# Optimization experiments

Measured on AMD Instinct MI355X. Metric: run time of the kernel, lower is better.

## Reference

```python
import jax, jax.numpy as jnp
import numpy as np

N_NODES = 50000
N_EDGES = 800000
IN_DIM = 128
EDGE_DIM = 32
HID = 64


def _glorot(key, shape):
    fan_in, fan_out = shape[0], shape[1]
    lim = float(np.sqrt(6.0 / (fan_in + fan_out)))
    return jax.random.uniform(key, shape, jnp.float32, -lim, lim)


def setup_inputs() -> dict:
    key = jax.random.key(0)
    ks = jax.random.split(key, 16)
    x = jax.random.normal(ks[0], (N_NODES, IN_DIM), jnp.float32)
    edge_index = jax.random.randint(ks[1], (2, N_EDGES), 0, N_NODES, jnp.int64)
    edge_attr = jax.random.normal(ks[2], (N_EDGES, EDGE_DIM), jnp.float32)
    message = jax.random.normal(ks[3], (N_EDGES, HID), jnp.float32)
    return {
        "x": x,
        "edge_index": edge_index,
        "edge_attr": edge_attr,
        "message": message,
        "W_src": _glorot(ks[4], (IN_DIM, HID)),
        "W_dest": _glorot(ks[5], (IN_DIM, HID)),
        "W_edge": _glorot(ks[6], (EDGE_DIM, HID)),
        "attn_vec": _glorot(ks[7], (1, HID)),
        "mlp_w1": _glorot(ks[8], (2 * HID, HID)),
        "mlp_b1": jnp.zeros((HID,), jnp.float32),
        "bn1_g": jnp.ones((HID,), jnp.float32),
        "bn1_b": jnp.zeros((HID,), jnp.float32),
        "mlp_w2": _glorot(ks[9], (HID, HID)),
        "mlp_b2": jnp.zeros((HID,), jnp.float32),
        "bn2_g": jnp.ones((HID,), jnp.float32),
        "bn2_b": jnp.zeros((HID,), jnp.float32),
        "amlp_w": _glorot(ks[10], (HID, 1)),
        "amlp_b": jnp.zeros((1,), jnp.float32),
    }


def _batchnorm(h, g, b, eps=1e-5):
    mu = jnp.mean(h, axis=0)
    var = jnp.var(h, axis=0)  # biased, as torch BN training forward
    return (h - mu) * jax.lax.rsqrt(var + eps) * g + b


def _segment_softmax(scores, seg, num_segments):
    m = jax.ops.segment_max(scores, seg, num_segments=num_segments)
    m = jnp.where(jnp.isneginf(m), 0.0, m)
    e = jnp.exp(scores - m[seg])
    s = jax.ops.segment_sum(e, seg, num_segments=num_segments)
    return e / s[seg]


def _scatter_max0(vals, seg, num_segments):
    # torch_scatter reduce='max' fills empty segments with 0
    out = jax.ops.segment_max(vals, seg, num_segments=num_segments)
    return jnp.where(jnp.isneginf(out), 0.0, out)


def reference(x, edge_index, edge_attr, message, W_src, W_dest, W_edge, attn_vec,
              mlp_w1, mlp_b1, bn1_g, bn1_b, mlp_w2, mlp_b2, bn2_g, bn2_b,
              amlp_w, amlp_b):
    row, col = edge_index[0], edge_index[1]
    # attention scores per edge
    h = x[row] @ W_src + x[col] @ W_dest + edge_attr @ W_edge  # [E, H]
    scores = jax.nn.leaky_relu(h @ attn_vec[0], negative_slope=0.2)  # [E]
    attn = _segment_softmax(scores, col, N_NODES)  # [E]
    msg = message * attn[:, None]  # [E, H]
    fwd = _scatter_max0(msg, col, N_NODES)  # [N, H]
    bwd = _scatter_max0(msg, row, N_NODES)  # [N, H]
    out = jnp.concatenate([fwd, bwd], axis=1)  # [N, 2H]
    # node MLP (BatchNorm in training-stats mode, dropout disabled)
    h1 = jax.nn.relu(_batchnorm(out @ mlp_w1 + mlp_b1, bn1_g, bn1_b))
    h2 = jax.nn.relu(_batchnorm(h1 @ mlp_w2 + mlp_b2, bn2_g, bn2_b))
    gate = jax.nn.sigmoid(h2 @ amlp_w + amlp_b).reshape(-1)  # [N]
    return h2, gate
```

## Files before the change

### kernel.cpp

```cpp
#include <hip/hip_runtime.h>
#include <hip/hip_bf16.h>
#include <float.h>

#define IN_DIM 128
#define EDGE_DIM 32
#define HID 64
#define BKT_G 64
#define BCAP 3072
#define NBKT_MAX 784
#define CHUNK 4096

__global__ void k_uvw(const float* __restrict__ Wsrc, const float* __restrict__ Wdst,
                      const float* __restrict__ Wedge, const float* __restrict__ avec,
                      const int* __restrict__ ei32, int* sflag,
                      float* u, float* v, float* w,
                      int* gcur, float* stats, int nbkt) {
    int gt = blockIdx.x * blockDim.x + threadIdx.x;
    int gstride = gridDim.x * blockDim.x;
    for (int i = gt; i < 2 * nbkt; i += gstride) gcur[i] = 0;
    for (int i = gt; i < 512; i += gstride) stats[i] = 0.0f;
    if (gt == 0) {
        int odd_or = ei32[1] | ei32[3] | ei32[5] | ei32[7] | ei32[9] | ei32[11];
        sflag[0] = (odd_or == 0) ? 2 : 1;
    }
    int wave = gt >> 6;
    int lane = threadIdx.x & 63;
    const float* src; float* dst; int row;
    if (wave < 128)      { src = Wsrc;  dst = u; row = wave; }
    else if (wave < 256) { src = Wdst;  dst = v; row = wave - 128; }
    else if (wave < 288) { src = Wedge; dst = w; row = wave - 256; }
    else return;
    float acc = src[row * HID + lane] * avec[lane];
    for (int o = 32; o >= 1; o >>= 1) acc += __shfl_xor(acc, o);
    if (lane == 0) dst[row] = acc;
}

__global__ void k_pqdot(const float* __restrict__ x, const float* __restrict__ u,
                        const float* __restrict__ v,
                        const float* __restrict__ ea, const float* __restrict__ w,
                        float* p, float* q, float* rdot, int N, int E, int pqBlocks) {
    if ((int)blockIdx.x < pqBlocks) {
        int wave = (blockIdx.x * blockDim.x + threadIdx.x) >> 6;
        int lane = threadIdx.x & 63;
        if (wave >= N) return;
        const float* xr = x + (size_t)wave * IN_DIM;
        float a0 = xr[lane], a1 = xr[lane + 64];
        float pp = a0 * u[lane] + a1 * u[lane + 64];
        float qq = a0 * v[lane] + a1 * v[lane + 64];
        for (int m = 32; m >= 1; m >>= 1) { pp += __shfl_xor(pp, m); qq += __shfl_xor(qq, m); }
        if (lane == 0) { p[wave] = pp; q[wave] = qq; }
    } else {
        int gid = (blockIdx.x - pqBlocks) * blockDim.x + threadIdx.x;
        int e = gid >> 3;
        int j = gid & 7;
        if (e >= E) return;
        float4 av = ((const float4*)ea)[(size_t)e * 8 + j];
        float4 wv = ((const float4*)w)[j];
        float val = av.x * wv.x + av.y * wv.y + av.z * wv.z + av.w * wv.w;
        val += __shfl_xor(val, 4);
        val += __shfl_xor(val, 2);
        val += __shfl_xor(val, 1);
        if (j == 0) rdot[e] = val;
    }
}

__global__ __launch_bounds__(256) void k_binscore(const int* __restrict__ ei,
                                                  const int* __restrict__ sflag,
                                                  const float* __restrict__ rdot,
                                                  const float* __restrict__ p,
                                                  const float* __restrict__ q,
                                                  float* scores,
                                                  int* gcur_col, int* gcur_row,
                                                  unsigned* bbuf_col, unsigned* bbuf_row,
                                                  int E, int nbkt) {
    __shared__ int lc[NBKT_MAX], lrw[NBKT_MAX];
    __shared__ int gc[NBKT_MAX], grw[NBKT_MAX];
    int tid = threadIdx.x;
    int e0 = blockIdx.x * CHUNK;
    int e1 = e0 + CHUNK; if (e1 > E) e1 = E;
    for (int i = tid; i < nbkt; i += 256) { lc[i] = 0; lrw[i] = 0; }
    __syncthreads();
    int st = sflag[0];
    for (int e = e0 + tid; e < e1; e += 256) {
        int r = ei[(size_t)st * e];
        int c = ei[(size_t)st * (E + e)];
        float sc = rdot[e] + p[r] + q[c];
        scores[e] = (sc > 0.f) ? sc : 0.2f * sc;
        atomicAdd(&lc[c >> 6], 1);
        atomicAdd(&lrw[r >> 6], 1);
    }
    __syncthreads();
    for (int b = tid; b < nbkt; b += 256) {
        int n1 = lc[b];  if (n1) gc[b]  = atomicAdd(&gcur_col[b], n1);
        int n2 = lrw[b]; if (n2) grw[b] = atomicAdd(&gcur_row[b], n2);
        lc[b] = 0; lrw[b] = 0;
    }
    __syncthreads();
    for (int e = e0 + tid; e < e1; e += 256) {
        int r = ei[(size_t)st * e];
        int c = ei[(size_t)st * (E + e)];
        int pos = gc[c >> 6] + atomicAdd(&lc[c >> 6], 1);
        if (pos < BCAP) bbuf_col[(size_t)(c >> 6) * BCAP + pos] = (unsigned)((e << 6) | (c & 63));
        int pos2 = grw[r >> 6] + atomicAdd(&lrw[r >> 6], 1);
        if (pos2 < BCAP) bbuf_row[(size_t)(r >> 6) * BCAP + pos2] = (unsigned)((e << 6) | (r & 63));
    }
}

__global__ __launch_bounds__(512) void k_sortfwd(float* scores, const float* __restrict__ msg,
                                                 const int* __restrict__ bcur,
                                                 const unsigned* __restrict__ bbuf,
                                                 float* fwd, int N) {
    __shared__ unsigned raw[BCAP];
    __shared__ unsigned srt[BCAP];
    __shared__ float    ssc[BCAP];
    __shared__ int cnt[BKT_G], cur[BKT_G], sstart[BKT_G + 1];
    int b = blockIdx.x, tid = threadIdx.x;
    int M = bcur[b]; if (M > BCAP) M = BCAP;
    if (tid < BKT_G) cnt[tid] = 0;
    __syncthreads();
    for (int i = tid; i < M; i += 512) {
        unsigned v = bbuf[(size_t)b * BCAP + i];
        raw[i] = v;
        atomicAdd(&cnt[v & 63], 1);
    }
    __syncthreads();
    if (tid < BKT_G) {
        int val = cnt[tid];
        int inc = val;
        for (int off = 1; off < BKT_G; off <<= 1) {
            int o = __shfl_up(inc, off);
            if (tid >= off) inc += o;
        }
        sstart[tid + 1] = inc;
        if (tid == 0) sstart[0] = 0;
        cur[tid] = inc - val;
    }
    __syncthreads();
    for (int j = tid; j < M; j += 512) {
        unsigned v = raw[j];
        int posn = atomicAdd(&cur[v & 63], 1);
        srt[posn] = v;
    }
    __syncthreads();
    for (int i = tid; i < M; i += 512) ssc[i] = scores[srt[i] >> 6];
    __syncthreads();
    int wave = tid >> 6, lane = tid & 63;
    for (int n = wave; n < BKT_G; n += 8) {
        int node = b * BKT_G + n;
        if (node >= N) continue;
        int a0 = sstart[n], len = sstart[n + 1] - a0;
        if (len == 0) { fwd[(size_t)node * HID + lane] = 0.f; continue; }
        float m = -FLT_MAX;
        for (int k = lane; k < len; k += 64) m = fmaxf(m, ssc[a0 + k]);
        for (int o = 32; o >= 1; o >>= 1) m = fmaxf(m, __shfl_xor(m, o));
        float ssum = 0.f;
        for (int k = lane; k < len; k += 64) ssum += expf(ssc[a0 + k] - m);
        for (int o = 32; o >= 1; o >>= 1) ssum += __shfl_xor(ssum, o);
        float rcp = 1.f / ssum;
        for (int k = lane; k < len; k += 64) {
            int i = a0 + k;
            float at = expf(ssc[i] - m) * rcp;
            ssc[i] = at;
            scores[srt[i] >> 6] = at;
        }
        asm volatile("s_waitcnt lgkmcnt(0)" ::: "memory");
        float acc = -FLT_MAX;
        int k = 0;
        for (; k + 8 <= len; k += 8) {
            float vv[8];
#pragma unroll
            for (int u8 = 0; u8 < 8; u8++) {
                int i = a0 + k + u8;
                vv[u8] = msg[(size_t)(srt[i] >> 6) * HID + lane] * ssc[i];
            }
#pragma unroll
            for (int u8 = 0; u8 < 8; u8++) acc = fmaxf(acc, vv[u8]);
        }
        for (; k < len; k++) {
            int i = a0 + k;
            acc = fmaxf(acc, msg[(size_t)(srt[i] >> 6) * HID + lane] * ssc[i]);
        }
        fwd[(size_t)node * HID + lane] = acc;
    }
}

__global__ __launch_bounds__(512) void k_sortbwd(const float* __restrict__ scores,
                                                 const float* __restrict__ msg,
                                                 const int* __restrict__ bcur,
                                                 const unsigned* __restrict__ bbuf,
                                                 float* bwd, int N) {
    __shared__ unsigned raw[BCAP];
    __shared__ unsigned srt[BCAP];
    __shared__ float    ssc[BCAP];
    __shared__ int cnt[BKT_G], cur[BKT_G], sstart[BKT_G + 1];
    int b = blockIdx.x, tid = threadIdx.x;
    int M = bcur[b]; if (M > BCAP) M = BCAP;
    if (tid < BKT_G) cnt[tid] = 0;
    __syncthreads();
    for (int i = tid; i < M; i += 512) {
        unsigned v = bbuf[(size_t)b * BCAP + i];
        raw[i] = v;
        atomicAdd(&cnt[v & 63], 1);
    }
    __syncthreads();
    if (tid < BKT_G) {
        int val = cnt[tid];
        int inc = val;
        for (int off = 1; off < BKT_G; off <<= 1) {
            int o = __shfl_up(inc, off);
            if (tid >= off) inc += o;
        }
        sstart[tid + 1] = inc;
        if (tid == 0) sstart[0] = 0;
        cur[tid] = inc - val;
    }
    __syncthreads();
    for (int j = tid; j < M; j += 512) {
        unsigned v = raw[j];
        int posn = atomicAdd(&cur[v & 63], 1);
        srt[posn] = v;
    }
    __syncthreads();
    for (int i = tid; i < M; i += 512) ssc[i] = scores[srt[i] >> 6];
    __syncthreads();
    int wave = tid >> 6, lane = tid & 63;
    for (int n = wave; n < BKT_G; n += 8) {
        int node = b * BKT_G + n;
        if (node >= N) continue;
        int a0 = sstart[n], len = sstart[n + 1] - a0;
        if (len == 0) { bwd[(size_t)node * HID + lane] = 0.f; continue; }
        float acc = -FLT_MAX;
        int k = 0;
        for (; k + 8 <= len; k += 8) {
            float vv[8];
#pragma unroll
            for (int u8 = 0; u8 < 8; u8++) {
                int i = a0 + k + u8;
                vv[u8] = msg[(size_t)(srt[i] >> 6) * HID + lane] * ssc[i];
            }
#pragma unroll
            for (int u8 = 0; u8 < 8; u8++) acc = fmaxf(acc, vv[u8]);
        }
        for (; k < len; k++) {
            int i = a0 + k;
            acc = fmaxf(acc, msg[(size_t)(srt[i] >> 6) * HID + lane] * ssc[i]);
        }
        bwd[(size_t)node * HID + lane] = acc;
    }
}

__global__ __launch_bounds__(256) void k_mlp1(const float* __restrict__ fwd,
                                              const float* __restrict__ bwd,
                                              const float* __restrict__ W1,
                                              const float* __restrict__ b1,
                                              float* pre1, float* gsum, float* gss, int N) {
    __shared__ float lsum[HID], lss[HID];
    int t = threadIdx.x;
    if (t < HID) { lsum[t] = 0.f; lss[t] = 0.f; }
    __syncthreads();
    int h = t & 63, lr = t >> 6;
    float bh = b1[h];
    float s = 0.f, ssq = 0.f;
    for (int n = blockIdx.x * 4 + lr; n < N; n += gridDim.x * 4) {
        const float* fr = fwd + (size_t)n * HID;
        const float* br = bwd + (size_t)n * HID;
        float a0 = bh, a1 = 0.f, a2 = 0.f, a3 = 0.f;
#pragma unroll
        for (int k = 0; k < HID; k += 4) {
            a0 += fr[k]     * W1[k * HID + h];
            a1 += fr[k + 1] * W1[(k + 1) * HID + h];
            a2 += fr[k + 2] * W1[(k + 2) * HID + h];
            a3 += fr[k + 3] * W1[(k + 3) * HID + h];
        }
#pragma unroll
        for (int k = 0; k < HID; k += 4) {
            a0 += br[k]     * W1[(HID + k) * HID + h];
            a1 += br[k + 1] * W1[(HID + k + 1) * HID + h];
            a2 += br[k + 2] * W1[(HID + k + 2) * HID + h];
            a3 += br[k + 3] * W1[(HID + k + 3) * HID + h];
        }
        float acc = (a0 + a1) + (a2 + a3);
        pre1[(size_t)n * HID + h] = acc;
        s += acc; ssq += acc * acc;
    }
    atomicAdd(&lsum[h], s);
    atomicAdd(&lss[h], ssq);
    __syncthreads();
    if (t < HID) { atomicAdd(&gsum[t], lsum[t]); atomicAdd(&gss[t], lss[t]); }
}

__global__ __launch_bounds__(256) void k_mlp2(const float* __restrict__ pre1,
                                              const float* __restrict__ gsum1,
                                              const float* __restrict__ gss1,
                                              const float* __restrict__ g1,
                                              const float* __restrict__ bb1,
                                              const float* __restrict__ W2,
                                              const float* __restrict__ b2v,
                                              float* pre2, float* gsum, float* gss, int N) {
    __shared__ float lsum[HID], lss[HID];
    __shared__ float sc1[HID], sh1[HID];
    int t = threadIdx.x;
    if (t < HID) {
        lsum[t] = 0.f; lss[t] = 0.f;
        float invN = 1.0f / (float)N;
        float mu = gsum1[t] * invN;
        float var = gss1[t] * invN - mu * mu;
        float rs = rsqrtf(var + 1e-5f);
        float s1 = rs * g1[t];
        sc1[t] = s1;
        sh1[t] = bb1[t] - mu * s1;
    }
    __syncthreads();
    int h = t & 63, lr = t >> 6;
    float bh = b2v[h];
    float s = 0.f, ssq = 0.f;
    for (int n = blockIdx.x * 4 + lr; n < N; n += gridDim.x * 4) {
        const float* pr = pre1 + (size_t)n * HID;
        float a0 = bh, a1 = 0.f, a2 = 0.f, a3 = 0.f;
#pragma unroll
        for (int k = 0; k < HID; k += 4) {
            float z0 = pr[k]     * sc1[k]     + sh1[k];     z0 = (z0 > 0.f) ? z0 : 0.f;
            float z1 = pr[k + 1] * sc1[k + 1] + sh1[k + 1]; z1 = (z1 > 0.f) ? z1 : 0.f;
            float z2 = pr[k + 2] * sc1[k + 2] + sh1[k + 2]; z2 = (z2 > 0.f) ? z2 : 0.f;
            float z3 = pr[k + 3] * sc1[k + 3] + sh1[k + 3]; z3 = (z3 > 0.f) ? z3 : 0.f;
            a0 += z0 * W2[k * HID + h];
            a1 += z1 * W2[(k + 1) * HID + h];
            a2 += z2 * W2[(k + 2) * HID + h];
            a3 += z3 * W2[(k + 3) * HID + h];
        }
        float acc = (a0 + a1) + (a2 + a3);
        pre2[(size_t)n * HID + h] = acc;
        s += acc; ssq += acc * acc;
    }
    atomicAdd(&lsum[h], s);
    atomicAdd(&lss[h], ssq);
    __syncthreads();
    if (t < HID) { atomicAdd(&gsum[t], lsum[t]); atomicAdd(&gss[t], lss[t]); }
}

__global__ __launch_bounds__(256) void k_out(const float* __restrict__ pre2,
                                             const float* __restrict__ gsum2,
                                             const float* __restrict__ gss2,
                                             const float* __restrict__ g2,
                                             const float* __restrict__ bb2,
                                             const float* __restrict__ amw,
                                             const float* __restrict__ amb,
                                             float* out, int N) {
    __shared__ float sc2[HID], sh2[HID];
    int t = threadIdx.x;
    if (t < HID) {
        float invN = 1.0f / (float)N;
        float mu = gsum2[t] * invN;
        float var = gss2[t] * invN - mu * mu;
        float rs = rsqrtf(var + 1e-5f);
        float s2 = rs * g2[t];
        sc2[t] = s2;
        sh2[t] = bb2[t] - mu * s2;
    }
    __syncthreads();
    int gid = blockIdx.x * blockDim.x + t;
    int n = gid >> 6, h = gid & 63;
    if (n >= N) return;
    float z = pre2[(size_t)n * HID + h] * sc2[h] + sh2[h];
    float h2 = (z > 0.f) ? z : 0.f;
    out[(size_t)n * HID + h] = h2;
    float part = h2 * amw[h];
    for (int m = 32; m >= 1; m >>= 1) part += __shfl_xor(part, m);
    if (h == 0) {
        float gate = 1.0f / (1.0f + expf(-(part + amb[0])));
        out[(size_t)N * HID + n] = gate;
    }
}

extern "C" void kernel_launch(void* const* d_in, const int* in_sizes, int n_in,
                              void* d_out, int out_size, void* d_ws, size_t ws_size,
                              hipStream_t stream) {
    const float* x     = (const float*)d_in[0];
    const int*   ei    = (const int*)d_in[1];
    const float* ea    = (const float*)d_in[2];
    const float* msg   = (const float*)d_in[3];
    const float* Wsrc  = (const float*)d_in[4];
    const float* Wdst  = (const float*)d_in[5];
    const float* Wedge = (const float*)d_in[6];
    const float* avec  = (const float*)d_in[7];
    const float* W1    = (const float*)d_in[8];
    const float* b1    = (const float*)d_in[9];
    const float* g1    = (const float*)d_in[10];
    const float* bb1   = (const float*)d_in[11];
    const float* W2    = (const float*)d_in[12];
    const float* b2    = (const float*)d_in[13];
    const float* g2    = (const float*)d_in[14];
    const float* bb2   = (const float*)d_in[15];
    const float* amw   = (const float*)d_in[16];
    const float* amb   = (const float*)d_in[17];
    float* out = (float*)d_out;

    const int N = in_sizes[0] / IN_DIM;
    const int E = in_sizes[1] / 2;
    const int NH = N * HID;
    const int nbkt = (N + BKT_G - 1) / BKT_G;

    float* ws = (float*)d_ws;
    float* gsum1  = ws;
    float* gss1   = ws + 64;
    float* gsum2  = ws + 128;
    float* gss2   = ws + 192;
    int*   sflag  = (int*)(ws + 512);
    float* u      = ws + 576;
    float* v      = ws + 704;
    float* w      = ws + 832;
    float* T        = ws + 1024;
    float* p        = T;
    float* q        = p + N;
    float* scores   = q + N;
    float* rdot     = scores + E;
    int*   gcur_col = (int*)(rdot + E);
    int*   gcur_row = gcur_col + nbkt;
    unsigned* bbuf_col = (unsigned*)(gcur_row + nbkt);
    unsigned* bbuf_row = bbuf_col + (size_t)nbkt * BCAP;
    size_t T_words  = 2 * (size_t)N + 2 * (size_t)E + 2 * (size_t)nbkt
                    + 2 * (size_t)nbkt * BCAP;
    size_t T_sz     = (T_words < (size_t)NH) ? (size_t)NH : T_words;
    float* fwd  = ws + 1024 + T_sz;
    float* bwd  = fwd + (size_t)NH;
    float* pre1 = T;
    float* pre2 = fwd;

    const int pqBlocks   = (N * 64 + 255) / 256;
    const int edotBlocks = (E * 8 + 255) / 256;

    hipLaunchKernelGGL(k_uvw, dim3(72), dim3(256), 0, stream,
                       Wsrc, Wdst, Wedge, avec, ei, sflag, u, v, w,
                       gcur_col, ws, nbkt);
    hipLaunchKernelGGL(k_pqdot, dim3(pqBlocks + edotBlocks), dim3(256), 0, stream,
                       x, u, v, ea, w, p, q, rdot, N, E, pqBlocks);
    hipLaunchKernelGGL(k_binscore, dim3((E + CHUNK - 1) / CHUNK), dim3(256), 0, stream,
                       ei, sflag, rdot, p, q, scores,
                       gcur_col, gcur_row, bbuf_col, bbuf_row, E, nbkt);
    hipLaunchKernelGGL(k_sortfwd, dim3(nbkt), dim3(512), 0, stream,
                       scores, msg, gcur_col, bbuf_col, fwd, N);
    hipLaunchKernelGGL(k_sortbwd, dim3(nbkt), dim3(512), 0, stream,
                       scores, msg, gcur_row, bbuf_row, bwd, N);
    hipLaunchKernelGGL(k_mlp1, dim3(1024), dim3(256), 0, stream,
                       fwd, bwd, W1, b1, pre1, gsum1, gss1, N);
    hipLaunchKernelGGL(k_mlp2, dim3(1024), dim3(256), 0, stream,
                       pre1, gsum1, gss1, g1, bb1, W2, b2, pre2, gsum2, gss2, N);
    hipLaunchKernelGGL(k_out, dim3(pqBlocks), dim3(256), 0, stream,
                       pre2, gsum2, gss2, g2, bb2, amw, amb, out, N);
}
```

Before: 307.8 us.

## Replace per-node sequential max with LDS atomicMax accumulation over bucket edges

The scatter-max in the forward and backward kernels now walks all edges of a 64-node bucket in a flat, wave-strided loop. It accumulates per-node maxima in a shared-memory array with order-preserving float-to-uint encoding and atomicMax, instead of each wave walking one node's sorted edge list. This removes load imbalance from variable node degree and drops the local counting sort in the backward kernel. In exchange it adds LDS atomics, which may contend, plus 16KB more shared memory per block, which can lower occupancy.

Measured after the change: 322.4 us. +4.8%, slower.

```diff
diff --git a/kernel.cpp b/kernel.cpp
--- a/kernel.cpp
+++ b/kernel.cpp
@@ -9,6 +9,16 @@
 #define BCAP 3072
 #define NBKT_MAX 784
 #define CHUNK 4096
+#define ENC_NEG_INF 0x007FFFFFu
+
+__device__ __forceinline__ unsigned encf(float f) {
+    unsigned u = __float_as_uint(f);
+    return (u & 0x80000000u) ? ~u : (u | 0x80000000u);
+}
+__device__ __forceinline__ float dec0(unsigned u) {
+    if (u == ENC_NEG_INF) return 0.0f;
+    return (u & 0x80000000u) ? __uint_as_float(u ^ 0x80000000u) : __uint_as_float(~u);
+}
 
 __global__ void k_uvw(const float* __restrict__ Wsrc, const float* __restrict__ Wdst,
                       const float* __restrict__ Wedge, const float* __restrict__ avec,
@@ -113,6 +123,7 @@
     __shared__ unsigned raw[BCAP];
     __shared__ unsigned srt[BCAP];
     __shared__ float    ssc[BCAP];
+    __shared__ unsigned facc[BKT_G * HID];
     __shared__ int cnt[BKT_G], cur[BKT_G], sstart[BKT_G + 1];
     int b = blockIdx.x, tid = threadIdx.x;
     int M = bcur[b]; if (M > BCAP) M = BCAP;
@@ -123,6 +134,7 @@
         raw[i] = v;
         atomicAdd(&cnt[v & 63], 1);
     }
+    for (int i = tid; i < BKT_G * HID; i += 512) facc[i] = ENC_NEG_INF;
     __syncthreads();
     if (tid < BKT_G) {
         int val = cnt[tid];
@@ -146,10 +158,8 @@
     __syncthreads();
     int wave = tid >> 6, lane = tid & 63;
     for (int n = wave; n < BKT_G; n += 8) {
-        int node = b * BKT_G + n;
-        if (node >= N) continue;
         int a0 = sstart[n], len = sstart[n + 1] - a0;
-        if (len == 0) { fwd[(size_t)node * HID + lane] = 0.f; continue; }
+        if (len == 0) continue;
         float m = -FLT_MAX;
         for (int k = lane; k < len; k += 64) m = fmaxf(m, ssc[a0 + k]);
         for (int o = 32; o >= 1; o >>= 1) m = fmaxf(m, __shfl_xor(m, o));
@@ -163,24 +173,30 @@
             ssc[i] = at;
             scores[srt[i] >> 6] = at;
         }
-        asm volatile("s_waitcnt lgkmcnt(0)" ::: "memory");
-        float acc = -FLT_MAX;
-        int k = 0;
-        for (; k + 8 <= len; k += 8) {
-            float vv[8];
-#pragma unroll
-            for (int u8 = 0; u8 < 8; u8++) {
-                int i = a0 + k + u8;
-                vv[u8] = msg[(size_t)(srt[i] >> 6) * HID + lane] * ssc[i];
-            }
-#pragma unroll
-            for (int u8 = 0; u8 < 8; u8++) acc = fmaxf(acc, vv[u8]);
-        }
-        for (; k < len; k++) {
-            int i = a0 + k;
-            acc = fmaxf(acc, msg[(size_t)(srt[i] >> 6) * HID + lane] * ssc[i]);
-        }
-        fwd[(size_t)node * HID + lane] = acc;
+    }
+    __syncthreads();
+    int i = wave;
+    for (; i + 24 < M; i += 32) {
+        unsigned s0 = srt[i], s1 = srt[i + 8], s2 = srt[i + 16], s3 = srt[i + 24];
+        float a0 = ssc[i], a1 = ssc[i + 8], a2 = ssc[i + 16], a3 = ssc[i + 24];
+        float v0 = msg[(size_t)(s0 >> 6) * HID + lane] * a0;
+        float v1 = msg[(size_t)(s1 >> 6) * HID + lane] * a1;
+        float v2 = msg[(size_t)(s2 >> 6) * HID + lane] * a2;
+        float v3 = msg[(size_t)(s3 >> 6) * HID + lane] * a3;
+        atomicMax(&facc[(s0 & 63) * HID + lane], encf(v0));
+        atomicMax(&facc[(s1 & 63) * HID + lane], encf(v1));
+        atomicMax(&facc[(s2 & 63) * HID + lane], encf(v2));
+        atomicMax(&facc[(s3 & 63) * HID + lane], encf(v3));
+    }
+    for (; i < M; i += 8) {
+        unsigned s0 = srt[i];
+        float v0 = msg[(size_t)(s0 >> 6) * HID + lane] * ssc[i];
+        atomicMax(&facc[(s0 & 63) * HID + lane], encf(v0));
+    }
+    __syncthreads();
+    for (int idx = tid; idx < BKT_G * HID; idx += 512) {
+        int node = b * BKT_G + (idx >> 6);
+        if (node < N) fwd[(size_t)node * HID + (idx & 63)] = dec0(facc[idx]);
     }
 }
 
@@ -190,62 +206,38 @@
                                                  const unsigned* __restrict__ bbuf,
                                                  float* bwd, int N) {
     __shared__ unsigned raw[BCAP];
-    __shared__ unsigned srt[BCAP];
     __shared__ float    ssc[BCAP];
-    __shared__ int cnt[BKT_G], cur[BKT_G], sstart[BKT_G + 1];
+    __shared__ unsigned facc[BKT_G * HID];
     int b = blockIdx.x, tid = threadIdx.x;
     int M = bcur[b]; if (M > BCAP) M = BCAP;
-    if (tid < BKT_G) cnt[tid] = 0;
-    __syncthreads();
-    for (int i = tid; i < M; i += 512) {
-        unsigned v = bbuf[(size_t)b * BCAP + i];
-        raw[i] = v;
-        atomicAdd(&cnt[v & 63], 1);
-    }
-    __syncthreads();
-    if (tid < BKT_G) {
-        int val = cnt[tid];
-        int inc = val;
-        for (int off = 1; off < BKT_G; off <<= 1) {
-            int o = __shfl_up(inc, off);
-            if (tid >= off) inc += o;
-        }
-        sstart[tid + 1] = inc;
-        if (tid == 0) sstart[0] = 0;
-        cur[tid] = inc - val;
-    }
-    __syncthreads();
-    for (int j = tid; j < M; j += 512) {
-        unsigned v = raw[j];
-        int posn = atomicAdd(&cur[v & 63], 1);
-        srt[posn] = v;
-    }
-    __syncthreads();
-    for (int i = tid; i < M; i += 512) ssc[i] = scores[srt[i] >> 6];
+    for (int i = tid; i < M; i += 512) raw[i] = bbuf[(size_t)b * BCAP + i];
+    for (int i = tid; i < BKT_G * HID; i += 512) facc[i] = ENC_NEG_INF;
+    __syncthreads();
+    for (int i = tid; i < M; i += 512) ssc[i] = scores[raw[i] >> 6];
     __syncthreads();
     int wave = tid >> 6, lane = tid & 63;
-    for (int n = wave; n < BKT_G; n += 8) {
-        int node = b * BKT_G + n;
-        if (node >= N) continue;
-        int a0 = sstart[n], len = sstart[n + 1] - a0;
-        if (len == 0) { bwd[(size_t)node * HID + lane] = 0.f; continue; }
-        float acc = -FLT_MAX;
-        int k = 0;
-        for (; k + 8 <= len; k += 8) {
-            float vv[8];
-#pragma unroll
-            for (int u8 = 0; u8 < 8; u8++) {
-                int i = a0 + k + u8;
-                vv[u8] = msg[(size_t)(srt[i] >> 6) * HID + lane] * ssc[i];
-            }
-#pragma unroll
-            for (int u8 = 0; u8 < 8; u8++) acc = fmaxf(acc, vv[u8]);
-        }
-        for (; k < len; k++) {
-            int i = a0 + k;
-            acc = fmaxf(acc, msg[(size_t)(srt[i] >> 6) * HID + lane] * ssc[i]);
-        }
-        bwd[(size_t)node * HID + lane] = acc;
+    int i = wave;
+    for (; i + 24 < M; i += 32) {
+        unsigned s0 = raw[i], s1 = raw[i + 8], s2 = raw[i + 16], s3 = raw[i + 24];
+        float a0 = ssc[i], a1 = ssc[i + 8], a2 = ssc[i + 16], a3 = ssc[i + 24];
+        float v0 = msg[(size_t)(s0 >> 6) * HID + lane] * a0;
+        float v1 = msg[(size_t)(s1 >> 6) * HID + lane] * a1;
+        float v2 = msg[(size_t)(s2 >> 6) * HID + lane] * a2;
+        float v3 = msg[(size_t)(s3 >> 6) * HID + lane] * a3;
+        atomicMax(&facc[(s0 & 63) * HID + lane], encf(v0));
+        atomicMax(&facc[(s1 & 63) * HID + lane], encf(v1));
+        atomicMax(&facc[(s2 & 63) * HID + lane], encf(v2));
+        atomicMax(&facc[(s3 & 63) * HID + lane], encf(v3));
+    }
+    for (; i < M; i += 8) {
+        unsigned s0 = raw[i];
+        float v0 = msg[(size_t)(s0 >> 6) * HID + lane] * ssc[i];
+        atomicMax(&facc[(s0 & 63) * HID + lane], encf(v0));
+    }
+    __syncthreads();
+    for (int idx = tid; idx < BKT_G * HID; idx += 512) {
+        int node = b * BKT_G + (idx >> 6);
+        if (node < N) bwd[(size_t)node * HID + (idx & 63)] = dec0(facc[idx]);
     }
 }
 
```
